# Kernel tuning notes

Measured on AMD Instinct MI355X. Metric: run time of the kernel, lower is better.

## Reference

```python
import jax, jax.numpy as jnp
import numpy as np

NEG_SLOPE = 0.2  # PyG GATv2Conv default leaky_relu negative slope


def _gatv2_layer(x, src, dst, n, Wl, bl, Wr, br, att, bias, concat):
    # PyG GATv2Conv (share_weights=False, edge_dim=None):
    #   x_l = lin_l(x) on source, x_r = lin_r(x) on target
    #   m = leaky_relu(x_l[src] + x_r[dst]); alpha = softmax_dst(<m, att>)
    #   out[i] = sum_{e: dst=i} alpha_e * x_l[src_e]
    H, C = att.shape
    xl = (x @ Wl + bl).reshape(n, H, C)
    xr = (x @ Wr + br).reshape(n, H, C)
    m = jax.nn.leaky_relu(xl[src] + xr[dst], NEG_SLOPE)      # [E,H,C]
    logits = jnp.einsum('ehc,hc->eh', m, att)                # [E,H]
    lmax = jax.ops.segment_max(logits, dst, num_segments=n)  # [N,H]
    e = jnp.exp(logits - lmax[dst])
    denom = jax.ops.segment_sum(e, dst, num_segments=n)
    alpha = e / (denom[dst] + 1e-16)                         # [E,H]
    out = jax.ops.segment_sum(xl[src] * alpha[:, :, None], dst, num_segments=n)
    out = out.reshape(n, H * C) if concat else out.mean(axis=1)
    return out + bias


def _glorot(key, shape):
    fan_in, fan_out = shape[0], shape[-1]
    s = jnp.sqrt(6.0 / (fan_in + fan_out))
    return jax.random.uniform(key, shape, jnp.float32, -s, s)


def setup_inputs() -> dict:
    key = jax.random.key(0)
    N, E, B = 50000, 800000, 512
    node_in, hidden, heads, meta_dim = 128, 32, 4, 12
    ks = jax.random.split(key, 32)
    inp = {
        'x': jax.random.normal(ks[0], (N, node_in), jnp.float32),
        'edge_index': jax.random.randint(ks[1], (2, E), 0, N, jnp.int64),
        'batch': jnp.sort(jax.random.randint(ks[2], (N,), 0, B, jnp.int64)),
        'metadata': jax.random.normal(ks[3], (B, meta_dim), jnp.float32),
    }
    dims = [(node_in, hidden, heads), (hidden * heads, hidden, heads), (hidden * heads, hidden, 1)]
    i = 4
    for li, (din, dh, H) in enumerate(dims):
        inp[f'Wl{li}'] = _glorot(ks[i], (din, H * dh)); i += 1
        inp[f'bl{li}'] = jnp.zeros((H * dh,), jnp.float32)
        inp[f'Wr{li}'] = _glorot(ks[i], (din, H * dh)); i += 1
        inp[f'br{li}'] = jnp.zeros((H * dh,), jnp.float32)
        inp[f'att{li}'] = _glorot(ks[i], (H, dh)); i += 1
        out_dim = H * dh if li < 2 else dh  # last layer concat=False
        inp[f'b{li}'] = jnp.zeros((out_dim,), jnp.float32)
    pool_dim = hidden  # n_layers=3 -> final single-head layer
    inp['Wh1'] = _glorot(ks[i], (pool_dim + meta_dim, pool_dim)); i += 1
    inp['bh1'] = jnp.zeros((pool_dim,), jnp.float32)
    inp['Wh2'] = _glorot(ks[i], (pool_dim, 1)); i += 1
    inp['bh2'] = jnp.zeros((1,), jnp.float32)
    return inp


def reference(x, edge_index, batch, metadata,
              Wl0, bl0, Wr0, br0, att0, b0,
              Wl1, bl1, Wr1, br1, att1, b1,
              Wl2, bl2, Wr2, br2, att2, b2,
              Wh1, bh1, Wh2, bh2):
    n = x.shape[0]
    B = metadata.shape[0]
    # PyG GATv2Conv add_self_loops=True
    loop = jnp.arange(n, dtype=edge_index.dtype)
    src = jnp.concatenate([edge_index[0], loop])
    dst = jnp.concatenate([edge_index[1], loop])
    params = [(Wl0, bl0, Wr0, br0, att0, b0, True),
              (Wl1, bl1, Wr1, br1, att1, b1, True),
              (Wl2, bl2, Wr2, br2, att2, b2, False)]
    h = x
    for (Wl, bl, Wr, br, att, bias, concat) in params:
        h = _gatv2_layer(h, src, dst, n, Wl, bl, Wr, br, att, bias, concat)
        h = jax.nn.elu(h)  # dropout is identity in eval mode
    # global mean pool over graphs
    sums = jax.ops.segment_sum(h, batch, num_segments=B)
    cnt = jax.ops.segment_sum(jnp.ones((n,), h.dtype), batch, num_segments=B)
    emb = sums / jnp.clip(cnt, 1.0)[:, None]
    z = jnp.concatenate([emb, metadata], axis=1)
    z = jax.nn.relu(z @ Wh1 + bh1)
    return z @ Wh2 + bh2  # (B, 1) logits
```

## Files before the change

kernel.cpp:

```cpp
#include <hip/hip_runtime.h>
#include <cstdint>
#include <cstddef>

#define NEG_SLOPE 0.2f
#define LOG2E 1.44269504f

typedef __attribute__((ext_vector_type(8))) short short8;
typedef __attribute__((ext_vector_type(4))) float f32x4;

__device__ __forceinline__ float bf2f(unsigned short u) {
    union { unsigned int i; float f; } x; x.i = ((unsigned int)u) << 16; return x.f;
}
__device__ __forceinline__ unsigned short f2bf(float f) {
    union { float f; unsigned int i; } x;
    x.f = f;
    unsigned int u = x.i;
    return (unsigned short)((u + 0x7FFFu + ((u >> 16) & 1u)) >> 16);
}

__global__ __launch_bounds__(256) void prep_w(
    const float* __restrict__ Wl, const float* __restrict__ Wr,
    int dout, unsigned short* __restrict__ Bt)
{
    int idx = blockIdx.x * 256 + threadIdx.x;
    int nTot = 2 * dout;
    if (idx >= nTot * 128) return;
    int n = idx >> 7, k = idx & 127;
    float v = (n < dout) ? Wl[(size_t)k * dout + n] : Wr[(size_t)k * dout + (n - dout)];
    Bt[idx] = f2bf(v);
}

__global__ __launch_bounds__(256) void gemm_mfma(
    const float* __restrict__ A, int M,
    const unsigned short* __restrict__ Bt,
    const float* __restrict__ bl, const float* __restrict__ br,
    int dout, unsigned short* __restrict__ XL, float* __restrict__ XR)
{
    constexpr int LDA = 136;
    __shared__ __attribute__((aligned(16))) unsigned short As[64 * LDA];
    __shared__ __attribute__((aligned(16))) unsigned short Bs[64 * LDA];
    const int t  = threadIdx.x;
    const int m0 = blockIdx.x * 64;
    const int n0 = blockIdx.y * 64;

#pragma unroll
    for (int i = 0; i < 8; ++i) {
        int c    = t + i * 256;
        int row  = c >> 5;
        int colc = (c & 31) * 4;
        int gr   = m0 + row;
        float4 v = make_float4(0.f, 0.f, 0.f, 0.f);
        if (gr < M) v = *(const float4*)(A + (size_t)gr * 128 + colc);
        ushort4 o;
        o.x = f2bf(v.x); o.y = f2bf(v.y); o.z = f2bf(v.z); o.w = f2bf(v.w);
        *(ushort4*)(As + row * LDA + colc) = o;
    }
#pragma unroll
    for (int i = 0; i < 4; ++i) {
        int c  = t + i * 256;
        int n  = c >> 4;
        int kc = (c & 15) * 8;
        *(short8*)(Bs + n * LDA + kc) =
            *(const short8*)(Bt + (size_t)(n0 + n) * 128 + kc);
    }
    __syncthreads();

    const int w    = t >> 6;
    const int lane = t & 63;
    const int fr   = lane & 15;
    const int quad = lane >> 4;

    f32x4 acc[4] = {};
    const unsigned short* ap  = As + (w * 16 + fr) * LDA + quad * 8;
    const unsigned short* bp0 = Bs + fr * LDA + quad * 8;
#pragma unroll
    for (int k0 = 0; k0 < 128; k0 += 32) {
        short8 afr = *(const short8*)(ap + k0);
#pragma unroll
        for (int j = 0; j < 4; ++j) {
            short8 bfr = *(const short8*)(bp0 + j * 16 * LDA + k0);
            acc[j] = __builtin_amdgcn_mfma_f32_16x16x32_bf16(afr, bfr, acc[j], 0, 0, 0);
        }
    }

#pragma unroll
    for (int j = 0; j < 4; ++j) {
        int col = n0 + j * 16 + fr;
        float bias = (col < dout) ? bl[col] : br[col - dout];
#pragma unroll
        for (int r = 0; r < 4; ++r) {
            int row = m0 + w * 16 + quad * 4 + r;
            if (row < M) {
                float v = acc[j][r] + bias;
                if (col < dout) XL[(size_t)row * dout + col] = f2bf(v);
                else            XR[(size_t)row * dout + (col - dout)] = v;
            }
        }
    }
}

__global__ void count_rank_kernel(const int* __restrict__ dst, int E,
                                  int* __restrict__ cnt, unsigned short* __restrict__ rank)
{
    int e = blockIdx.x * blockDim.x + threadIdx.x;
    if (e < E) {
        int p = atomicAdd(&cnt[dst[e]], 1);
        rank[e] = (unsigned short)p;
    }
}

__global__ __launch_bounds__(256) void scan_partial(
    const int* __restrict__ cnt, int N, int* __restrict__ bsum)
{
    __shared__ int red[4];
    const int t = threadIdx.x;
    const int base = blockIdx.x * 2048;
    int s = 0;
#pragma unroll
    for (int i = 0; i < 8; ++i) {
        int idx = base + t + i * 256;
        if (idx < N) s += cnt[idx];
    }
#pragma unroll
    for (int off = 32; off >= 1; off >>= 1) s += __shfl_xor(s, off);
    if ((t & 63) == 0) red[t >> 6] = s;
    __syncthreads();
    if (t == 0) bsum[blockIdx.x] = red[0] + red[1] + red[2] + red[3];
}

__global__ __launch_bounds__(256) void scan_bsums(
    int* __restrict__ bsum, int nb, int E, int* __restrict__ rowptr, int N)
{
    __shared__ int sh[256];
    const int t = threadIdx.x;
    int v = (t < nb) ? bsum[t] : 0;
    sh[t] = v;
    __syncthreads();
    for (int off = 1; off < 256; off <<= 1) {
        int u = (t >= off) ? sh[t - off] : 0;
        __syncthreads();
        sh[t] += u;
        __syncthreads();
    }
    if (t < nb) bsum[t] = sh[t] - v;
    if (t == 0) rowptr[N] = E;
}

__global__ __launch_bounds__(256) void scan_final(
    const int* __restrict__ cnt, int N, const int* __restrict__ bsum,
    int* __restrict__ rowptr)
{
    __shared__ int sdat[2048];
    __shared__ int tsum[256];
    const int t = threadIdx.x;
    const int base = blockIdx.x * 2048;
#pragma unroll
    for (int i = 0; i < 8; ++i) {
        int idx = base + t + i * 256;
        sdat[t + i * 256] = (idx < N) ? cnt[idx] : 0;
    }
    __syncthreads();
    int vals[8];
    int s = 0;
#pragma unroll
    for (int j = 0; j < 8; ++j) { vals[j] = sdat[t * 8 + j]; s += vals[j]; }
    tsum[t] = s;
    __syncthreads();
    for (int off = 1; off < 256; off <<= 1) {
        int u = (t >= off) ? tsum[t - off] : 0;
        __syncthreads();
        tsum[t] += u;
        __syncthreads();
    }
    int run = bsum[blockIdx.x] + tsum[t] - s;
#pragma unroll
    for (int j = 0; j < 8; ++j) { sdat[t * 8 + j] = run; run += vals[j]; }
    __syncthreads();
#pragma unroll
    for (int i = 0; i < 8; ++i) {
        int idx = base + t + i * 256;
        if (idx < N) rowptr[idx] = sdat[t + i * 256];
    }
}

__global__ void place_kernel(const int* __restrict__ src, const int* __restrict__ dst,
                             const unsigned short* __restrict__ rank, int E,
                             const int* __restrict__ rowptr,
                             unsigned short* __restrict__ csr_src)
{
    int e = blockIdx.x * blockDim.x + threadIdx.x;
    if (e < E)
        csr_src[rowptr[dst[e]] + rank[e]] = (unsigned short)src[e];
}

template<int H>
__global__ __launch_bounds__(256, 4) void gat_fused(
    const unsigned short* __restrict__ xl, const float* __restrict__ xr,
    const int* __restrict__ rowptr, const unsigned short* __restrict__ csr_src,
    const float* __restrict__ att, const float* __restrict__ bias,
    float* __restrict__ hout, int hstride, int N)
{
    constexpr int HC  = 32 * H;
    constexpr int LPE = HC / 4;
    constexpr int EPW = 64 / LPE;
    const int node = blockIdx.x * 4 + (threadIdx.x >> 6);
    if (node >= N) return;
    const int lane = threadIdx.x & 63;
    const int q    = lane % LPE;
    const int slot = lane / LPE;
    const int rs   = rowptr[node];
    const int re   = rowptr[node + 1];

    const unsigned short* __restrict__ xlb = xl + 4 * q;
    const float4 xri = *(const float4*)(xr + (size_t)node * HC + 4 * q);
    float4 a6 = *(const float4*)(att + 4 * q);
    float4 a4;
    a4.x = a6.x * (0.4f * LOG2E); a4.y = a6.y * (0.4f * LOG2E);
    a4.z = a6.z * (0.4f * LOG2E); a4.w = a6.w * (0.4f * LOG2E);
    a6.x *= 0.6f * LOG2E; a6.y *= 0.6f * LOG2E;
    a6.z *= 0.6f * LOG2E; a6.w *= 0.6f * LOG2E;

    float l = 0.f;
    float4 acc = make_float4(0.f, 0.f, 0.f, 0.f);

    auto ld4 = [&](int s) -> float4 {
        ushort4 u = *(const ushort4*)(xlb + (size_t)s * HC);
        float4 v;
        v.x = bf2f(u.x); v.y = bf2f(u.y); v.z = bf2f(u.z); v.w = bf2f(u.w);
        return v;
    };

    auto edge_w = [&](const float4& v) -> float {
        float sx = v.x + xri.x, sy = v.y + xri.y, sz = v.z + xri.z, sw = v.w + xri.w;
        float p0 = a6.x * sx;
        float p1 = a4.x * fabsf(sx);
        p0 = fmaf(a6.y, sy, p0);
        p1 = fmaf(a4.y, fabsf(sy), p1);
        p0 = fmaf(a6.z, sz, p0);
        p1 = fmaf(a4.z, fabsf(sz), p1);
        p0 = fmaf(a6.w, sw, p0);
        p1 = fmaf(a4.w, fabsf(sw), p1);
        float p = p0 + p1;
        p += __shfl_xor(p, 1);
        p += __shfl_xor(p, 2);
        p += __shfl_xor(p, 4);
        return exp2f(p);
    };

    if (slot == 0) {
        float4 v = ld4(node);
        float w = edge_w(v);
        l = w;
        acc.x = w * v.x; acc.y = w * v.y; acc.z = w * v.z; acc.w = w * v.w;
    }

    int k = rs + slot;
    for (; k + EPW < re; k += 2 * EPW) {
        int s0 = csr_src[k];
        int s1 = csr_src[k + EPW];
        float4 v0 = ld4(s0);
        float4 v1 = ld4(s1);
        float w0 = edge_w(v0);
        float w1 = edge_w(v1);
        l += w0 + w1;
        acc.x = fmaf(w0, v0.x, fmaf(w1, v1.x, acc.x));
        acc.y = fmaf(w0, v0.y, fmaf(w1, v1.y, acc.y));
        acc.z = fmaf(w0, v0.z, fmaf(w1, v1.z, acc.z));
        acc.w = fmaf(w0, v0.w, fmaf(w1, v1.w, acc.w));
    }
    if (k < re) {
        int s0 = csr_src[k];
        float4 v0 = ld4(s0);
        float w0 = edge_w(v0);
        l += w0;
        acc.x = fmaf(w0, v0.x, acc.x);
        acc.y = fmaf(w0, v0.y, acc.y);
        acc.z = fmaf(w0, v0.z, acc.z);
        acc.w = fmaf(w0, v0.w, acc.w);
    }

#pragma unroll
    for (int mask = LPE; mask < 64; mask <<= 1) {
        l     += __shfl_xor(l, mask);
        acc.x += __shfl_xor(acc.x, mask);
        acc.y += __shfl_xor(acc.y, mask);
        acc.z += __shfl_xor(acc.z, mask);
        acc.w += __shfl_xor(acc.w, mask);
    }

    if (lane < LPE) {
        const float4 bi = *(const float4*)(bias + 4 * q);
        float inv = 1.f / (l + 1e-16f);
        float4 o;
        o.x = acc.x * inv + bi.x;
        o.y = acc.y * inv + bi.y;
        o.z = acc.z * inv + bi.z;
        o.w = acc.w * inv + bi.w;
        o.x = (o.x > 0.f) ? o.x : expm1f(o.x);
        o.y = (o.y > 0.f) ? o.y : expm1f(o.y);
        o.z = (o.z > 0.f) ? o.z : expm1f(o.z);
        o.w = (o.w > 0.f) ? o.w : expm1f(o.w);
        *(float4*)(hout + (size_t)node * hstride + 4 * q) = o;
    }
}

__global__ __launch_bounds__(128) void pool_head_kernel(
    const float* __restrict__ h, int hstride,
    const int* __restrict__ batch, int N,
    const float* __restrict__ meta,
    const float* __restrict__ Wh1, const float* __restrict__ bh1,
    const float* __restrict__ Wh2, const float* __restrict__ bh2,
    float* __restrict__ out)
{
    const int b = blockIdx.x;
    const int t = threadIdx.x;
    __shared__ float s[128];
    __shared__ float z[44];

    int lo = 0, hi = N;
    while (lo < hi) { int mid = (lo + hi) >> 1; if (batch[mid] < b) lo = mid + 1; else hi = mid; }
    int lo2 = lo, hi2 = N;
    while (lo2 < hi2) { int mid = (lo2 + hi2) >> 1; if (batch[mid] < b + 1) lo2 = mid + 1; else hi2 = mid; }
    const int start = lo, end = lo2;

    const int c = t & 31, r = t >> 5;
    float acc = 0.f;
    for (int row = start + r; row < end; row += 4)
        acc += h[(size_t)row * hstride + c];
    s[t] = acc;
    __syncthreads();
    if (t < 32) {
        float sum = s[t] + s[t + 32] + s[t + 64] + s[t + 96];
        z[t] = sum / fmaxf((float)(end - start), 1.0f);
    } else if (t < 44) {
        z[t] = meta[(size_t)b * 12 + (t - 32)];
    }
    __syncthreads();
    if (t < 32) {
        float hj = bh1[t];
#pragma unroll
        for (int k = 0; k < 44; ++k)
            hj = fmaf(z[k], Wh1[k * 32 + t], hj);
        hj = fmaxf(hj, 0.f);
        float p = hj * Wh2[t];
#pragma unroll
        for (int off = 16; off >= 1; off >>= 1)
            p += __shfl_xor(p, off, 32);
        if (t == 0) out[b] = p + bh2[0];
    }
}

extern "C" void kernel_launch(void* const* d_in, const int* in_sizes, int n_in,
                              void* d_out, int out_size, void* d_ws, size_t ws_size,
                              hipStream_t stream)
{
    const float* x     = (const float*)d_in[0];
    const int*   ei    = (const int*)d_in[1];
    const int*   batch = (const int*)d_in[2];
    const float* meta  = (const float*)d_in[3];
    const float* Wl[3]  = {(const float*)d_in[4],  (const float*)d_in[10], (const float*)d_in[16]};
    const float* bl[3]  = {(const float*)d_in[5],  (const float*)d_in[11], (const float*)d_in[17]};
    const float* Wr[3]  = {(const float*)d_in[6],  (const float*)d_in[12], (const float*)d_in[18]};
    const float* br[3]  = {(const float*)d_in[7],  (const float*)d_in[13], (const float*)d_in[19]};
    const float* att[3] = {(const float*)d_in[8],  (const float*)d_in[14], (const float*)d_in[20]};
    const float* bb[3]  = {(const float*)d_in[9],  (const float*)d_in[15], (const float*)d_in[21]};
    const float* Wh1 = (const float*)d_in[22];
    const float* bh1 = (const float*)d_in[23];
    const float* Wh2 = (const float*)d_in[24];
    const float* bh2 = (const float*)d_in[25];
    float* out = (float*)d_out;

    const int N  = in_sizes[0] / 128;
    const int E  = in_sizes[1] / 2;
    const int B  = in_sizes[3] / 12;
    const int NB = (N + 2047) / 2048;

    char* wsp = (char*)d_ws;
    size_t off_ = 0;
    auto alloc = [&](size_t bytes) {
        char* p = wsp + off_;
        off_ = (off_ + bytes + 255) & ~(size_t)255;
        return p;
    };
    unsigned short* xlbuf = (unsigned short*)alloc((size_t)N * 128 * 2);
    float* xrbuf   = (float*)alloc((size_t)N * 128 * 4);
    float* hbuf    = (float*)alloc((size_t)N * 128 * 4);
    int*   cnt     = (int*)alloc((size_t)N * 4);
    int*   rowptr  = (int*)alloc((size_t)(N + 1) * 4);
    unsigned short* rank    = (unsigned short*)alloc((size_t)E * 2);
    unsigned short* csr_src = (unsigned short*)alloc((size_t)E * 2);
    unsigned short* Bt      = (unsigned short*)alloc((size_t)256 * 128 * 2);
    int*   bsum    = (int*)alloc((size_t)256 * 4);

    const int* srcI = ei;
    const int* dstI = ei + E;

    hipMemsetAsync(cnt, 0, (size_t)N * 4, stream);
    count_rank_kernel<<<(E + 255) / 256, 256, 0, stream>>>(dstI, E, cnt, rank);
    scan_partial<<<NB, 256, 0, stream>>>(cnt, N, bsum);
    scan_bsums<<<1, 256, 0, stream>>>(bsum, NB, E, rowptr, N);
    scan_final<<<NB, 256, 0, stream>>>(cnt, N, bsum, rowptr);
    place_kernel<<<(E + 255) / 256, 256, 0, stream>>>(srcI, dstI, rank, E, rowptr, csr_src);

    const int GB = (N + 3) / 4;
    const int MB = (N + 63) / 64;

    {
        prep_w<<<(2 * 128 * 128 + 255) / 256, 256, 0, stream>>>(Wl[0], Wr[0], 128, Bt);
        gemm_mfma<<<dim3(MB, 4), 256, 0, stream>>>(x, N, Bt, bl[0], br[0], 128, xlbuf, xrbuf);
        gat_fused<4><<<GB, 256, 0, stream>>>(xlbuf, xrbuf, rowptr, csr_src, att[0], bb[0], hbuf, 128, N);
    }
    {
        prep_w<<<(2 * 128 * 128 + 255) / 256, 256, 0, stream>>>(Wl[1], Wr[1], 128, Bt);
        gemm_mfma<<<dim3(MB, 4), 256, 0, stream>>>(hbuf, N, Bt, bl[1], br[1], 128, xlbuf, xrbuf);
        gat_fused<4><<<GB, 256, 0, stream>>>(xlbuf, xrbuf, rowptr, csr_src, att[1], bb[1], hbuf, 128, N);
    }
    {
        prep_w<<<(2 * 32 * 128 + 255) / 256, 256, 0, stream>>>(Wl[2], Wr[2], 32, Bt);
        gemm_mfma<<<dim3(MB, 1), 256, 0, stream>>>(hbuf, N, Bt, bl[2], br[2], 32, xlbuf, xrbuf);
        gat_fused<1><<<GB, 256, 0, stream>>>(xlbuf, xrbuf, rowptr, csr_src, att[2], bb[2], hbuf, 32, N);
    }
    pool_head_kernel<<<B, 128, 0, stream>>>(hbuf, 32, batch, N, meta, Wh1, bh1, Wh2, bh2, out);
}
```

Before: 402.9 us.

## Merge weight prep launches, double GEMM M-tile, use packed float2 math in GAT

Merges the three per-layer weight transpose/convert launches into one kernel that writes three separate bf16 buffers up front, which removes two launches. The MFMA GEMM now covers 128 rows per block, so each B fragment read from LDS feeds two MFMAs and fewer blocks are launched. The GAT edge loop is rewritten with f32x2 vector arithmetic so the compiler can emit packed FP32 ops, and bf16 values are unpacked from 32-bit words. The larger LDS tile (about 52KB) may reduce occupancy in the GEMM.

```diff
diff --git a/kernel.cpp b/kernel.cpp
--- a/kernel.cpp
+++ b/kernel.cpp
@@ -7,9 +7,13 @@
 
 typedef __attribute__((ext_vector_type(8))) short short8;
 typedef __attribute__((ext_vector_type(4))) float f32x4;
-
-__device__ __forceinline__ float bf2f(unsigned short u) {
-    union { unsigned int i; float f; } x; x.i = ((unsigned int)u) << 16; return x.f;
+typedef __attribute__((ext_vector_type(2))) float f32x2;
+
+__device__ __forceinline__ float bflo(unsigned int u) {
+    union { unsigned int i; float f; } x; x.i = u << 16; return x.f;
+}
+__device__ __forceinline__ float bfhi(unsigned int u) {
+    union { unsigned int i; float f; } x; x.i = u & 0xFFFF0000u; return x.f;
 }
 __device__ __forceinline__ unsigned short f2bf(float f) {
     union { float f; unsigned int i; } x;
@@ -18,13 +22,20 @@
     return (unsigned short)((u + 0x7FFFu + ((u >> 16) & 1u)) >> 16);
 }
 
-__global__ __launch_bounds__(256) void prep_w(
-    const float* __restrict__ Wl, const float* __restrict__ Wr,
-    int dout, unsigned short* __restrict__ Bt)
+__global__ __launch_bounds__(256) void prep_w_all(
+    const float* __restrict__ Wl0, const float* __restrict__ Wr0,
+    const float* __restrict__ Wl1, const float* __restrict__ Wr1,
+    const float* __restrict__ Wl2, const float* __restrict__ Wr2,
+    unsigned short* __restrict__ Bt0, unsigned short* __restrict__ Bt1,
+    unsigned short* __restrict__ Bt2)
 {
     int idx = blockIdx.x * 256 + threadIdx.x;
-    int nTot = 2 * dout;
-    if (idx >= nTot * 128) return;
+    const int SZ = 256 * 128;
+    const float *Wl, *Wr; unsigned short* Bt; int dout;
+    if (idx < SZ)              { Wl = Wl0; Wr = Wr0; Bt = Bt0; dout = 128; }
+    else if (idx < 2 * SZ)     { Wl = Wl1; Wr = Wr1; Bt = Bt1; dout = 128; idx -= SZ; }
+    else if (idx < 2 * SZ + 64 * 128) { Wl = Wl2; Wr = Wr2; Bt = Bt2; dout = 32; idx -= 2 * SZ; }
+    else return;
     int n = idx >> 7, k = idx & 127;
     float v = (n < dout) ? Wl[(size_t)k * dout + n] : Wr[(size_t)k * dout + (n - dout)];
     Bt[idx] = f2bf(v);
@@ -37,14 +48,14 @@
     int dout, unsigned short* __restrict__ XL, float* __restrict__ XR)
 {
     constexpr int LDA = 136;
-    __shared__ __attribute__((aligned(16))) unsigned short As[64 * LDA];
+    __shared__ __attribute__((aligned(16))) unsigned short As[128 * LDA];
     __shared__ __attribute__((aligned(16))) unsigned short Bs[64 * LDA];
     const int t  = threadIdx.x;
-    const int m0 = blockIdx.x * 64;
+    const int m0 = blockIdx.x * 128;
     const int n0 = blockIdx.y * 64;
 
 #pragma unroll
-    for (int i = 0; i < 8; ++i) {
+    for (int i = 0; i < 16; ++i) {
         int c    = t + i * 256;
         int row  = c >> 5;
         int colc = (c & 31) * 4;
@@ -70,16 +81,18 @@
     const int fr   = lane & 15;
     const int quad = lane >> 4;
 
-    f32x4 acc[4] = {};
-    const unsigned short* ap  = As + (w * 16 + fr) * LDA + quad * 8;
+    f32x4 acc[2][4] = {};
+    const unsigned short* ap0 = As + (w * 32 + fr) * LDA + quad * 8;
     const unsigned short* bp0 = Bs + fr * LDA + quad * 8;
 #pragma unroll
     for (int k0 = 0; k0 < 128; k0 += 32) {
-        short8 afr = *(const short8*)(ap + k0);
+        short8 afr0 = *(const short8*)(ap0 + k0);
+        short8 afr1 = *(const short8*)(ap0 + 16 * LDA + k0);
 #pragma unroll
         for (int j = 0; j < 4; ++j) {
             short8 bfr = *(const short8*)(bp0 + j * 16 * LDA + k0);
-            acc[j] = __builtin_amdgcn_mfma_f32_16x16x32_bf16(afr, bfr, acc[j], 0, 0, 0);
+            acc[0][j] = __builtin_amdgcn_mfma_f32_16x16x32_bf16(afr0, bfr, acc[0][j], 0, 0, 0);
+            acc[1][j] = __builtin_amdgcn_mfma_f32_16x16x32_bf16(afr1, bfr, acc[1][j], 0, 0, 0);
         }
     }
 
@@ -88,12 +101,15 @@
         int col = n0 + j * 16 + fr;
         float bias = (col < dout) ? bl[col] : br[col - dout];
 #pragma unroll
-        for (int r = 0; r < 4; ++r) {
-            int row = m0 + w * 16 + quad * 4 + r;
-            if (row < M) {
-                float v = acc[j][r] + bias;
-                if (col < dout) XL[(size_t)row * dout + col] = f2bf(v);
-                else            XR[(size_t)row * dout + (col - dout)] = v;
+        for (int i = 0; i < 2; ++i) {
+#pragma unroll
+            for (int r = 0; r < 4; ++r) {
+                int row = m0 + w * 32 + i * 16 + quad * 4 + r;
+                if (row < M) {
+                    float v = acc[i][j][r] + bias;
+                    if (col < dout) XL[(size_t)row * dout + col] = f2bf(v);
+                    else            XR[(size_t)row * dout + (col - dout)] = v;
+                }
             }
         }
     }
@@ -212,35 +228,40 @@
     const int re   = rowptr[node + 1];
 
     const unsigned short* __restrict__ xlb = xl + 4 * q;
-    const float4 xri = *(const float4*)(xr + (size_t)node * HC + 4 * q);
-    float4 a6 = *(const float4*)(att + 4 * q);
-    float4 a4;
-    a4.x = a6.x * (0.4f * LOG2E); a4.y = a6.y * (0.4f * LOG2E);
-    a4.z = a6.z * (0.4f * LOG2E); a4.w = a6.w * (0.4f * LOG2E);
-    a6.x *= 0.6f * LOG2E; a6.y *= 0.6f * LOG2E;
-    a6.z *= 0.6f * LOG2E; a6.w *= 0.6f * LOG2E;
+
+    f32x2 xr01, xr23, a6_01, a6_23, a4_01, a4_23;
+    {
+        const float4 xv = *(const float4*)(xr + (size_t)node * HC + 4 * q);
+        const float4 av = *(const float4*)(att + 4 * q);
+        xr01.x = xv.x; xr01.y = xv.y; xr23.x = xv.z; xr23.y = xv.w;
+        a6_01.x = av.x * (0.6f * LOG2E); a6_01.y = av.y * (0.6f * LOG2E);
+        a6_23.x = av.z * (0.6f * LOG2E); a6_23.y = av.w * (0.6f * LOG2E);
+        a4_01.x = av.x * (0.4f * LOG2E); a4_01.y = av.y * (0.4f * LOG2E);
+        a4_23.x = av.z * (0.4f * LOG2E); a4_23.y = av.w * (0.4f * LOG2E);
+    }
 
     float l = 0.f;
-    float4 acc = make_float4(0.f, 0.f, 0.f, 0.f);
-
-    auto ld4 = [&](int s) -> float4 {
-        ushort4 u = *(const ushort4*)(xlb + (size_t)s * HC);
-        float4 v;
-        v.x = bf2f(u.x); v.y = bf2f(u.y); v.z = bf2f(u.z); v.w = bf2f(u.w);
-        return v;
+    f32x2 ac01 = {0.f, 0.f}, ac23 = {0.f, 0.f};
+
+    struct V2 { f32x2 v01, v23; };
+    auto ld4 = [&](int s) -> V2 {
+        uint2 u = *(const uint2*)(xlb + (size_t)s * HC);
+        V2 r;
+        r.v01.x = bflo(u.x); r.v01.y = bfhi(u.x);
+        r.v23.x = bflo(u.y); r.v23.y = bfhi(u.y);
+        return r;
     };
 
-    auto edge_w = [&](const float4& v) -> float {
-        float sx = v.x + xri.x, sy = v.y + xri.y, sz = v.z + xri.z, sw = v.w + xri.w;
-        float p0 = a6.x * sx;
-        float p1 = a4.x * fabsf(sx);
-        p0 = fmaf(a6.y, sy, p0);
-        p1 = fmaf(a4.y, fabsf(sy), p1);
-        p0 = fmaf(a6.z, sz, p0);
-        p1 = fmaf(a4.z, fabsf(sz), p1);
-        p0 = fmaf(a6.w, sw, p0);
-        p1 = fmaf(a4.w, fabsf(sw), p1);
-        float p = p0 + p1;
+    auto edge_w = [&](const V2& v) -> float {
+        f32x2 s01 = v.v01 + xr01;
+        f32x2 s23 = v.v23 + xr23;
+        f32x2 t01 = __builtin_elementwise_abs(s01);
+        f32x2 t23 = __builtin_elementwise_abs(s23);
+        f32x2 p2 = s01 * a6_01;
+        p2 = __builtin_elementwise_fma(s23, a6_23, p2);
+        p2 = __builtin_elementwise_fma(t01, a4_01, p2);
+        p2 = __builtin_elementwise_fma(t23, a4_23, p2);
+        float p = p2.x + p2.y;
         p += __shfl_xor(p, 1);
         p += __shfl_xor(p, 2);
         p += __shfl_xor(p, 4);
@@ -248,54 +269,55 @@
     };
 
     if (slot == 0) {
-        float4 v = ld4(node);
+        V2 v = ld4(node);
         float w = edge_w(v);
         l = w;
-        acc.x = w * v.x; acc.y = w * v.y; acc.z = w * v.z; acc.w = w * v.w;
+        f32x2 wv; wv.x = w; wv.y = w;
+        ac01 = wv * v.v01;
+        ac23 = wv * v.v23;
     }
 
     int k = rs + slot;
     for (; k + EPW < re; k += 2 * EPW) {
         int s0 = csr_src[k];
         int s1 = csr_src[k + EPW];
-        float4 v0 = ld4(s0);
-        float4 v1 = ld4(s1);
+        V2 v0 = ld4(s0);
+        V2 v1 = ld4(s1);
         float w0 = edge_w(v0);
         float w1 = edge_w(v1);
         l += w0 + w1;
-        acc.x = fmaf(w0, v0.x, fmaf(w1, v1.x, acc.x));
-        acc.y = fmaf(w0, v0.y, fmaf(w1, v1.y, acc.y));
-        acc.z = fmaf(w0, v0.z, fmaf(w1, v1.z, acc.z));
-        acc.w = fmaf(w0, v0.w, fmaf(w1, v1.w, acc.w));
+        f32x2 w0v; w0v.x = w0; w0v.y = w0;
+        f32x2 w1v; w1v.x = w1; w1v.y = w1;
+        ac01 = __builtin_elementwise_fma(w0v, v0.v01, __builtin_elementwise_fma(w1v, v1.v01, ac01));
+        ac23 = __builtin_elementwise_fma(w0v, v0.v23, __builtin_elementwise_fma(w1v, v1.v23, ac23));
     }
     if (k < re) {
         int s0 = csr_src[k];
-        float4 v0 = ld4(s0);
+        V2 v0 = ld4(s0);
         float w0 = edge_w(v0);
         l += w0;
-        acc.x = fmaf(w0, v0.x, acc.x);
-        acc.y = fmaf(w0, v0.y, acc.y);
-        acc.z = fmaf(w0, v0.z, acc.z);
-        acc.w = fmaf(w0, v0.w, acc.w);
+        f32x2 w0v; w0v.x = w0; w0v.y = w0;
+        ac01 = __builtin_elementwise_fma(w0v, v0.v01, ac01);
+        ac23 = __builtin_elementwise_fma(w0v, v0.v23, ac23);
     }
 
 #pragma unroll
     for (int mask = LPE; mask < 64; mask <<= 1) {
-        l     += __shfl_xor(l, mask);
-        acc.x += __shfl_xor(acc.x, mask);
-        acc.y += __shfl_xor(acc.y, mask);
-        acc.z += __shfl_xor(acc.z, mask);
-        acc.w += __shfl_xor(acc.w, mask);
+        l      += __shfl_xor(l, mask);
+        ac01.x += __shfl_xor(ac01.x, mask);
+        ac01.y += __shfl_xor(ac01.y, mask);
+        ac23.x += __shfl_xor(ac23.x, mask);
+        ac23.y += __shfl_xor(ac23.y, mask);
     }
 
     if (lane < LPE) {
         const float4 bi = *(const float4*)(bias + 4 * q);
         float inv = 1.f / (l + 1e-16f);
         float4 o;
-        o.x = acc.x * inv + bi.x;
-        o.y = acc.y * inv + bi.y;
-        o.z = acc.z * inv + bi.z;
-        o.w = acc.w * inv + bi.w;
+        o.x = ac01.x * inv + bi.x;
+        o.y = ac01.y * inv + bi.y;
+        o.z = ac23.x * inv + bi.z;
+        o.w = ac23.y * inv + bi.w;
         o.x = (o.x > 0.f) ? o.x : expm1f(o.x);
         o.y = (o.y > 0.f) ? o.y : expm1f(o.y);
         o.z = (o.z > 0.f) ? o.z : expm1f(o.z);
@@ -389,11 +411,16 @@
     int*   rowptr  = (int*)alloc((size_t)(N + 1) * 4);
     unsigned short* rank    = (unsigned short*)alloc((size_t)E * 2);
     unsigned short* csr_src = (unsigned short*)alloc((size_t)E * 2);
-    unsigned short* Bt      = (unsigned short*)alloc((size_t)256 * 128 * 2);
+    unsigned short* Bt0     = (unsigned short*)alloc((size_t)256 * 128 * 2);
+    unsigned short* Bt1     = (unsigned short*)alloc((size_t)256 * 128 * 2);
+    unsigned short* Bt2     = (unsigned short*)alloc((size_t)64 * 128 * 2);
     int*   bsum    = (int*)alloc((size_t)256 * 4);
 
     const int* srcI = ei;
     const int* dstI = ei + E;
+
+    prep_w_all<<<(2 * 256 * 128 + 64 * 128 + 255) / 256, 256, 0, stream>>>(
+        Wl[0], Wr[0], Wl[1], Wr[1], Wl[2], Wr[2], Bt0, Bt1, Bt2);
 
     hipMemsetAsync(cnt, 0, (size_t)N * 4, stream);
     count_rank_kernel<<<(E + 255) / 256, 256, 0, stream>>>(dstI, E, cnt, rank);
@@ -403,21 +430,18 @@
     place_kernel<<<(E + 255) / 256, 256, 0, stream>>>(srcI, dstI, rank, E, rowptr, csr_src);
 
     const int GB = (N + 3) / 4;
-    const int MB = (N + 63) / 64;
+    const int MB = (N + 127) / 128;
 
     {
-        prep_w<<<(2 * 128 * 128 + 255) / 256, 256, 0, stream>>>(Wl[0], Wr[0], 128, Bt);
-        gemm_mfma<<<dim3(MB, 4), 256, 0, stream>>>(x, N, Bt, bl[0], br[0], 128, xlbuf, xrbuf);
+        gemm_mfma<<<dim3(MB, 4), 256, 0, stream>>>(x, N, Bt0, bl[0], br[0], 128, xlbuf, xrbuf);
         gat_fused<4><<<GB, 256, 0, stream>>>(xlbuf, xrbuf, rowptr, csr_src, att[0], bb[0], hbuf, 128, N);
     }
     {
-        prep_w<<<(2 * 128 * 128 + 255) / 256, 256, 0, stream>>>(Wl[1], Wr[1], 128, Bt);
-        gemm_mfma<<<dim3(MB, 4), 256, 0, stream>>>(hbuf, N, Bt, bl[1], br[1], 128, xlbuf, xrbuf);
+        gemm_mfma<<<dim3(MB, 4), 256, 0, stream>>>(hbuf, N, Bt1, bl[1], br[1], 128, xlbuf, xrbuf);
         gat_fused<4><<<GB, 256, 0, stream>>>(xlbuf, xrbuf, rowptr, csr_src, att[1], bb[1], hbuf, 128, N);
     }
     {
-        prep_w<<<(2 * 32 * 128 + 255) / 256, 256, 0, stream>>>(Wl[2], Wr[2], 32, Bt);
-        gemm_mfma<<<dim3(MB, 1), 256, 0, stream>>>(hbuf, N, Bt, bl[2], br[2], 32, xlbuf, xrbuf);
+        gemm_mfma<<<dim3(MB, 1), 256, 0, stream>>>(hbuf, N, Bt2, bl[2], br[2], 32, xlbuf, xrbuf);
         gat_fused<1><<<GB, 256, 0, stream>>>(xlbuf, xrbuf, rowptr, csr_src, att[2], bb[2], hbuf, 32, N);
     }
     pool_head_kernel<<<B, 128, 0, stream>>>(hbuf, 32, batch, N, meta, Wh1, bh1, Wh2, bh2, out);
```

After: 409.6 us. No clear change (+1.7%).
